# Kernel tuning notes

Measured on AMD Instinct MI355X. Metric: run time of the kernel, lower is better.

## Reference

```python
import jax, jax.numpy as jnp
import numpy as np

NUM_HEADS = 32
NUM_KV_HEADS = 8
HEAD_DIM = 64

def rotate_half(x):
    x1, x2 = jnp.split(x, 2, axis=-1)
    return jnp.concatenate((-x2, x1), axis=-1)

def setup_inputs() -> dict:
    key = jax.random.key(0)
    ks = jax.random.split(key, 7)
    B, S, H = 1, 2048, 2048
    hidden_states = jax.random.normal(ks[0], (B, S, H), dtype=jnp.float32)
    # RoPE tables (llama-style) for positions 0..S-1
    inv_freq = 1.0 / (10000.0 ** (np.arange(0, HEAD_DIM, 2, dtype=np.float32) / HEAD_DIM))
    t = np.arange(S, dtype=np.float32)
    freqs = np.outer(t, inv_freq)              # [S, HEAD_DIM//2]
    emb = np.concatenate([freqs, freqs], axis=-1)  # [S, HEAD_DIM]
    cos = jnp.asarray(np.cos(emb)[None], dtype=jnp.float32)  # [1, S, HEAD_DIM]
    sin = jnp.asarray(np.sin(emb)[None], dtype=jnp.float32)
    sc = 0.02
    Wq = jax.random.normal(ks[1], (H, H), dtype=jnp.float32) * sc
    Wk = jax.random.normal(ks[2], (NUM_KV_HEADS * HEAD_DIM, H), dtype=jnp.float32) * sc
    Wv = jax.random.normal(ks[3], (NUM_KV_HEADS * HEAD_DIM, H), dtype=jnp.float32) * sc
    Wo = jax.random.normal(ks[4], (H, H), dtype=jnp.float32) * sc
    return {"hidden_states": hidden_states, "cos": cos, "sin": sin,
            "Wq": Wq, "Wk": Wk, "Wv": Wv, "Wo": Wo}

def reference(hidden_states, cos, sin, Wq, Wk, Wv, Wo):
    B, S, H = hidden_states.shape
    nh, nkv, hd = NUM_HEADS, NUM_KV_HEADS, HEAD_DIM
    n_rep = nh // nkv
    # projections (torch Linear: x @ W.T)
    q = (hidden_states @ Wq.T).reshape(B, S, nh, hd).transpose(0, 2, 1, 3)   # [B,nh,S,hd]
    k = (hidden_states @ Wk.T).reshape(B, S, nkv, hd).transpose(0, 2, 1, 3)  # [B,nkv,S,hd]
    v = (hidden_states @ Wv.T).reshape(B, S, nkv, hd).transpose(0, 2, 1, 3)
    # RoPE: cos/sin [B,S,hd] -> broadcast over heads
    c = cos[:, None, :, :]
    s = sin[:, None, :, :]
    q = q * c + rotate_half(q) * s
    k = k * c + rotate_half(k) * s
    # GQA: repeat_interleave kv heads
    k = jnp.repeat(k, n_rep, axis=1)  # [B,nh,S,hd]
    v = jnp.repeat(v, n_rep, axis=1)
    # eager attention (NOTE: source applies no causal mask)
    scores = jnp.einsum('bhqd,bhkd->bhqk', q, k) / jnp.sqrt(jnp.float32(hd))
    attn = jax.nn.softmax(scores.astype(jnp.float32), axis=-1).astype(q.dtype)
    out = jnp.einsum('bhqk,bhkd->bhqd', attn, v)          # [B,nh,S,hd]
    out = out.transpose(0, 2, 1, 3).reshape(B, S, nh * hd)
    return out @ Wo.T
```

## Files before the change

### kernel.cpp

```cpp
#include <hip/hip_runtime.h>

typedef __bf16 bf16;
typedef __bf16 bf16x8 __attribute__((ext_vector_type(8)));
typedef __bf16 bf16x4 __attribute__((ext_vector_type(4)));
typedef float f32x4 __attribute__((ext_vector_type(4)));

__device__ __forceinline__ void gload_lds16(const void* g, void* l) {
  __builtin_amdgcn_global_load_lds(
      (const __attribute__((address_space(1))) void*)g,
      (__attribute__((address_space(3))) void*)l, 16, 0, 0);
}

__global__ __launch_bounds__(256) void cast_f32_bf16(const float* __restrict__ src,
                                                     bf16* __restrict__ dst, int n) {
  int i = (blockIdx.x * 256 + threadIdx.x) * 4;
  if (i >= n) return;
  float4 v = *(const float4*)(src + i);
  bf16x4 o;
  o[0] = (bf16)v.x; o[1] = (bf16)v.y; o[2] = (bf16)v.z; o[3] = (bf16)v.w;
  *(bf16x4*)(dst + i) = o;
}

__global__ __launch_bounds__(256) void gemm_qkv(const bf16* __restrict__ A,
                                                const bf16* __restrict__ B,
                                                bf16* __restrict__ QK,
                                                bf16* __restrict__ Vt_g,
                                                int K) {
  __shared__ bf16 As[128][64];
  __shared__ bf16 Bs[128][64];
  const int tid  = threadIdx.x;
  const int lane = tid & 63;
  const int w    = tid >> 6;
  const int m0 = blockIdx.y * 128;
  const int n0 = blockIdx.x * 128;
  const int wr = w >> 1, wc = w & 1;

  f32x4 acc[4][4] = {};

  const bf16* Ag = A + (long)(m0 + w * 32 + (lane >> 3)) * K + ((lane & 7) << 3);
  const bf16* Bg = B + (long)(n0 + w * 32 + (lane >> 3)) * K + ((lane & 7) << 3);

  for (int k0 = 0; k0 < K; k0 += 64) {
#pragma unroll
    for (int i = 0; i < 4; ++i) {
      gload_lds16(Ag + (long)i * 8 * K + k0, &As[w * 32 + i * 8][0]);
      gload_lds16(Bg + (long)i * 8 * K + k0, &Bs[w * 32 + i * 8][0]);
    }
    __syncthreads();
#pragma unroll
    for (int kk = 0; kk < 64; kk += 32) {
      bf16x8 a[4], b[4];
#pragma unroll
      for (int m = 0; m < 4; ++m)
        a[m] = *(const bf16x8*)&As[wr * 64 + m * 16 + (lane & 15)][kk + ((lane >> 4) << 3)];
#pragma unroll
      for (int n = 0; n < 4; ++n)
        b[n] = *(const bf16x8*)&Bs[wc * 64 + n * 16 + (lane & 15)][kk + ((lane >> 4) << 3)];
#pragma unroll
      for (int m = 0; m < 4; ++m)
#pragma unroll
        for (int n = 0; n < 4; ++n)
          acc[m][n] = __builtin_amdgcn_mfma_f32_16x16x32_bf16(a[m], b[n], acc[m][n], 0, 0, 0);
    }
    __syncthreads();
  }

  const int rb = m0 + wr * 64 + ((lane >> 4) << 2);
  const int cb = n0 + wc * 64 + (lane & 15);
  if (n0 >= 2560) {
#pragma unroll
    for (int m = 0; m < 4; ++m)
#pragma unroll
      for (int n = 0; n < 4; ++n)
#pragma unroll
        for (int j = 0; j < 4; ++j)
          Vt_g[(long)(cb + n * 16 - 2560) * 2048 + (rb + m * 16 + j)] = (bf16)acc[m][n][j];
  } else {
#pragma unroll
    for (int m = 0; m < 4; ++m)
#pragma unroll
      for (int n = 0; n < 4; ++n)
#pragma unroll
        for (int j = 0; j < 4; ++j)
          QK[(long)(rb + m * 16 + j) * 2560 + (cb + n * 16)] = (bf16)acc[m][n][j];
  }
}

__global__ __launch_bounds__(256) void gemm_bt_f32(const bf16* __restrict__ A,
                                                   const bf16* __restrict__ B,
                                                   float* __restrict__ C,
                                                   int K, int ldc) {
  __shared__ bf16 As[128][64];
  __shared__ bf16 Bs[128][64];
  const int tid  = threadIdx.x;
  const int lane = tid & 63;
  const int w    = tid >> 6;
  const int m0 = blockIdx.y * 128;
  const int n0 = blockIdx.x * 128;
  const int wr = w >> 1, wc = w & 1;

  f32x4 acc[4][4] = {};

  const bf16* Ag = A + (long)(m0 + w * 32 + (lane >> 3)) * K + ((lane & 7) << 3);
  const bf16* Bg = B + (long)(n0 + w * 32 + (lane >> 3)) * K + ((lane & 7) << 3);

  for (int k0 = 0; k0 < K; k0 += 64) {
#pragma unroll
    for (int i = 0; i < 4; ++i) {
      gload_lds16(Ag + (long)i * 8 * K + k0, &As[w * 32 + i * 8][0]);
      gload_lds16(Bg + (long)i * 8 * K + k0, &Bs[w * 32 + i * 8][0]);
    }
    __syncthreads();
#pragma unroll
    for (int kk = 0; kk < 64; kk += 32) {
      bf16x8 a[4], b[4];
#pragma unroll
      for (int m = 0; m < 4; ++m)
        a[m] = *(const bf16x8*)&As[wr * 64 + m * 16 + (lane & 15)][kk + ((lane >> 4) << 3)];
#pragma unroll
      for (int n = 0; n < 4; ++n)
        b[n] = *(const bf16x8*)&Bs[wc * 64 + n * 16 + (lane & 15)][kk + ((lane >> 4) << 3)];
#pragma unroll
      for (int m = 0; m < 4; ++m)
#pragma unroll
        for (int n = 0; n < 4; ++n)
          acc[m][n] = __builtin_amdgcn_mfma_f32_16x16x32_bf16(a[m], b[n], acc[m][n], 0, 0, 0);
    }
    __syncthreads();
  }

  const int rb = m0 + wr * 64 + ((lane >> 4) << 2);
  const int cb = n0 + wc * 64 + (lane & 15);
#pragma unroll
  for (int m = 0; m < 4; ++m)
#pragma unroll
    for (int n = 0; n < 4; ++n)
#pragma unroll
      for (int j = 0; j < 4; ++j)
        C[(long)(rb + m * 16 + j) * ldc + (cb + n * 16)] = acc[m][n][j];
}

__global__ __launch_bounds__(256) void rope_scale(bf16* __restrict__ QK,
                                                  const float* __restrict__ cosb,
                                                  const float* __restrict__ sinb) {
  int t = blockIdx.x * 256 + threadIdx.x;
  int s = t / 160;
  int rem = t - s * 160;
  int hh = rem >> 2;
  int d0 = (rem & 3) << 3;
  long base = (long)s * 2560 + hh * 64 + d0;
  bf16x8 lo = *(const bf16x8*)(QK + base);
  bf16x8 hi = *(const bf16x8*)(QK + base + 32);
  float4 c0 = *(const float4*)(cosb + s * 64 + d0);
  float4 c1 = *(const float4*)(cosb + s * 64 + d0 + 4);
  float4 s0 = *(const float4*)(sinb + s * 64 + d0);
  float4 s1 = *(const float4*)(sinb + s * 64 + d0 + 4);
  float cs[8] = {c0.x, c0.y, c0.z, c0.w, c1.x, c1.y, c1.z, c1.w};
  float sn[8] = {s0.x, s0.y, s0.z, s0.w, s1.x, s1.y, s1.z, s1.w};
  float scale = hh < 32 ? 0.125f : 1.0f;
  bf16x8 nlo, nhi;
#pragma unroll
  for (int i = 0; i < 8; ++i) {
    float L = (float)lo[i], H = (float)hi[i];
    nlo[i] = (bf16)((L * cs[i] - H * sn[i]) * scale);
    nhi[i] = (bf16)((H * cs[i] + L * sn[i]) * scale);
  }
  *(bf16x8*)(QK + base)      = nlo;
  *(bf16x8*)(QK + base + 32) = nhi;
}

__global__ __launch_bounds__(512) void attn_v2(const bf16* __restrict__ QK,
                                               const bf16* __restrict__ Vg,
                                               bf16* __restrict__ O) {
  constexpr int LDT = 72;
  __shared__ bf16 Kt[64][LDT];
  __shared__ bf16 Vt[64][LDT];
  __shared__ bf16 Pl[8][16][LDT];
  const int h   = blockIdx.y;
  const int q0  = blockIdx.x * 128;
  const int kvh = h >> 2;
  const int tid = threadIdx.x, lane = tid & 63, w = tid >> 6;
  const int l15 = lane & 15, lq = lane >> 4;

  const bf16* qptr = QK + (long)(q0 + w * 16 + l15) * 2560 + h * 64 + (lq << 3);
  bf16x8 qf[2];
  qf[0] = *(const bf16x8*)(qptr);
  qf[1] = *(const bf16x8*)(qptr + 32);

  const int sr = tid >> 3;
  const int sc = (tid & 7) << 3;
  const bf16* ksrc = QK + (long)sr * 2560 + 2048 + kvh * 64 + sc;
  const bf16* vsrc = Vg + (long)(kvh * 64 + sr) * 2048 + sc;

  f32x4 oacc[4] = {};
  float lrow[4] = {0.f, 0.f, 0.f, 0.f};

  bf16x8 kreg = *(const bf16x8*)ksrc;
  bf16x8 vreg = *(const bf16x8*)vsrc;

  for (int t = 0; t < 32; ++t) {
    *(bf16x8*)&Kt[sr][sc] = kreg;
    *(bf16x8*)&Vt[sr][sc] = vreg;
    __syncthreads();
    if (t != 31) {
      ksrc += 64 * 2560;
      vsrc += 64;
      kreg = *(const bf16x8*)ksrc;
      vreg = *(const bf16x8*)vsrc;
    }

    f32x4 sacc[4] = {};
#pragma unroll
    for (int kx = 0; kx < 2; ++kx)
#pragma unroll
      for (int nf = 0; nf < 4; ++nf) {
        bf16x8 b = *(const bf16x8*)&Kt[nf * 16 + l15][kx * 32 + (lq << 3)];
        sacc[nf] = __builtin_amdgcn_mfma_f32_16x16x32_bf16(qf[kx], b, sacc[nf], 0, 0, 0);
      }

#pragma unroll
    for (int nf = 0; nf < 4; ++nf)
#pragma unroll
      for (int j = 0; j < 4; ++j) {
        float pv = __expf(sacc[nf][j]);
        lrow[j] += pv;
        Pl[w][(lq << 2) + j][nf * 16 + l15] = (bf16)pv;
      }

#pragma unroll
    for (int kx = 0; kx < 2; ++kx) {
      bf16x8 a = *(const bf16x8*)&Pl[w][l15][kx * 32 + (lq << 3)];
#pragma unroll
      for (int nf = 0; nf < 4; ++nf) {
        bf16x8 b = *(const bf16x8*)&Vt[nf * 16 + l15][kx * 32 + (lq << 3)];
        oacc[nf] = __builtin_amdgcn_mfma_f32_16x16x32_bf16(a, b, oacc[nf], 0, 0, 0);
      }
    }
    __syncthreads();
  }

  float ls[4];
#pragma unroll
  for (int j = 0; j < 4; ++j) {
    float v = lrow[j];
#pragma unroll
    for (int off = 1; off < 16; off <<= 1) v += __shfl_xor(v, off, 64);
    ls[j] = v;
  }
#pragma unroll
  for (int nf = 0; nf < 4; ++nf)
#pragma unroll
    for (int j = 0; j < 4; ++j) {
      int r = q0 + w * 16 + (lq << 2) + j;
      int c = h * 64 + nf * 16 + l15;
      O[(long)r * 2048 + c] = (bf16)(oacc[nf][j] / ls[j]);
    }
}

extern "C" void kernel_launch(void* const* d_in, const int* in_sizes, int n_in,
                              void* d_out, int out_size, void* d_ws, size_t ws_size,
                              hipStream_t stream) {
  const float* hs   = (const float*)d_in[0];
  const float* cosb = (const float*)d_in[1];
  const float* sinb = (const float*)d_in[2];
  const float* Wq   = (const float*)d_in[3];
  const float* Wk   = (const float*)d_in[4];
  const float* Wv   = (const float*)d_in[5];
  const float* Wo   = (const float*)d_in[6];
  float* out = (float*)d_out;

  char* ws = (char*)d_ws;
  bf16* hsb   = (bf16*)(ws);
  bf16* Wqkv  = (bf16*)(ws + (8l  << 20));
  bf16* Wob   = (bf16*)(ws + (20l << 20));
  bf16* QKbuf = (bf16*)(ws + (28l << 20));
  bf16* Vt_g  = (bf16*)(ws + (38l << 20));
  bf16* AO    = (bf16*)(ws + (40l << 20));

  cast_f32_bf16<<<4096, 256, 0, stream>>>(hs, hsb, 4194304);
  cast_f32_bf16<<<4096, 256, 0, stream>>>(Wq, Wqkv, 4194304);
  cast_f32_bf16<<<1024, 256, 0, stream>>>(Wk, Wqkv + 2048l * 2048, 1048576);
  cast_f32_bf16<<<1024, 256, 0, stream>>>(Wv, Wqkv + 2560l * 2048, 1048576);
  cast_f32_bf16<<<4096, 256, 0, stream>>>(Wo, Wob, 4194304);

  gemm_qkv<<<dim3(24, 16), 256, 0, stream>>>(hsb, Wqkv, QKbuf, Vt_g, 2048);

  rope_scale<<<1280, 256, 0, stream>>>(QKbuf, cosb, sinb);

  attn_v2<<<dim3(16, 32), 512, 0, stream>>>(QKbuf, Vt_g, AO);

  gemm_bt_f32<<<dim3(16, 16), 256, 0, stream>>>(AO, Wob, out, 2048, 2048);
}
```

Before: 271.7 us.

## Fuse casts into one kernel, fold RoPE into QKV GEMM, double-buffer GEMM LDS

The five separate f32-to-bf16 cast launches become one kernel that picks its source and destination by index range. The RoPE and scale pass is moved into the QKV GEMM epilogue, which removes one launch and a read-modify-write of the QK buffer. Both GEMMs now double-buffer their LDS tiles so the next K-slice load is issued before the current slice's MFMAs. The cost is twice the LDS per block, which may lower occupancy, and scattered scalar cos/sin loads in the epilogue.

Measured after the change: 260.2 us. 1.04x faster.

```diff
diff --git a/kernel.cpp b/kernel.cpp
--- a/kernel.cpp
+++ b/kernel.cpp
@@ -11,51 +11,74 @@
       (__attribute__((address_space(3))) void*)l, 16, 0, 0);
 }
 
-__global__ __launch_bounds__(256) void cast_f32_bf16(const float* __restrict__ src,
-                                                     bf16* __restrict__ dst, int n) {
-  int i = (blockIdx.x * 256 + threadIdx.x) * 4;
-  if (i >= n) return;
-  float4 v = *(const float4*)(src + i);
+__global__ __launch_bounds__(256) void cast_all(const float* __restrict__ hs,
+                                                const float* __restrict__ Wq,
+                                                const float* __restrict__ Wk,
+                                                const float* __restrict__ Wv,
+                                                const float* __restrict__ Wo,
+                                                bf16* __restrict__ hsb,
+                                                bf16* __restrict__ Wqkv,
+                                                bf16* __restrict__ Wob) {
+  long i = (long)blockIdx.x * 256 + threadIdx.x;
+  const float* s; bf16* d;
+  if (i < 1048576)      { s = hs + i * 4;                 d = hsb  + i * 4; }
+  else if (i < 2097152) { s = Wq + (i - 1048576) * 4;     d = Wqkv + (i - 1048576) * 4; }
+  else if (i < 2359296) { s = Wk + (i - 2097152) * 4;     d = Wqkv + 4194304 + (i - 2097152) * 4; }
+  else if (i < 2621440) { s = Wv + (i - 2359296) * 4;     d = Wqkv + 5242880 + (i - 2359296) * 4; }
+  else                  { s = Wo + (i - 2621440) * 4;     d = Wob  + (i - 2621440) * 4; }
+  float4 v = *(const float4*)s;
   bf16x4 o;
   o[0] = (bf16)v.x; o[1] = (bf16)v.y; o[2] = (bf16)v.z; o[3] = (bf16)v.w;
-  *(bf16x4*)(dst + i) = o;
+  *(bf16x4*)d = o;
 }
 
 __global__ __launch_bounds__(256) void gemm_qkv(const bf16* __restrict__ A,
                                                 const bf16* __restrict__ B,
+                                                const float* __restrict__ cosb,
+                                                const float* __restrict__ sinb,
                                                 bf16* __restrict__ QK,
                                                 bf16* __restrict__ Vt_g,
                                                 int K) {
-  __shared__ bf16 As[128][64];
-  __shared__ bf16 Bs[128][64];
+  __shared__ bf16 As[2][128][64];
+  __shared__ bf16 Bs[2][128][64];
   const int tid  = threadIdx.x;
   const int lane = tid & 63;
   const int w    = tid >> 6;
   const int m0 = blockIdx.y * 128;
   const int n0 = blockIdx.x * 128;
   const int wr = w >> 1, wc = w & 1;
+  const int l15 = lane & 15, lq = lane >> 4;
 
   f32x4 acc[4][4] = {};
 
   const bf16* Ag = A + (long)(m0 + w * 32 + (lane >> 3)) * K + ((lane & 7) << 3);
   const bf16* Bg = B + (long)(n0 + w * 32 + (lane >> 3)) * K + ((lane & 7) << 3);
 
+#pragma unroll
+  for (int i = 0; i < 4; ++i) {
+    gload_lds16(Ag + (long)i * 8 * K, &As[0][w * 32 + i * 8][0]);
+    gload_lds16(Bg + (long)i * 8 * K, &Bs[0][w * 32 + i * 8][0]);
+  }
+  __syncthreads();
+
+  int cur = 0;
   for (int k0 = 0; k0 < K; k0 += 64) {
-#pragma unroll
-    for (int i = 0; i < 4; ++i) {
-      gload_lds16(Ag + (long)i * 8 * K + k0, &As[w * 32 + i * 8][0]);
-      gload_lds16(Bg + (long)i * 8 * K + k0, &Bs[w * 32 + i * 8][0]);
-    }
-    __syncthreads();
+    if (k0 + 64 < K) {
+#pragma unroll
+      for (int i = 0; i < 4; ++i) {
+        gload_lds16(Ag + (long)i * 8 * K + k0 + 64, &As[cur ^ 1][w * 32 + i * 8][0]);
+        gload_lds16(Bg + (long)i * 8 * K + k0 + 64, &Bs[cur ^ 1][w * 32 + i * 8][0]);
+      }
+    }
 #pragma unroll
     for (int kk = 0; kk < 64; kk += 32) {
       bf16x8 a[4], b[4];
 #pragma unroll
       for (int m = 0; m < 4; ++m)
-        a[m] = *(const bf16x8*)&As[wr * 64 + m * 16 + (lane & 15)][kk + ((lane >> 4) << 3)];
+        a[m] = *(const bf16x8*)&As[cur][wr * 64 + m * 16 + l15][kk + (lq << 3)];
 #pragma unroll
       for (int n = 0; n < 4; ++n)
-        b[n] = *(const bf16x8*)&Bs[wc * 64 + n * 16 + (lane & 15)][kk + ((lane >> 4) << 3)];
+        b[n] = *(const bf16x8*)&Bs[cur][wc * 64 + n * 16 + l15][kk + (lq << 3)];
 #pragma unroll
       for (int m = 0; m < 4; ++m)
 #pragma unroll
@@ -63,11 +86,12 @@
           acc[m][n] = __builtin_amdgcn_mfma_f32_16x16x32_bf16(a[m], b[n], acc[m][n], 0, 0, 0);
     }
     __syncthreads();
-  }
-
-  const int rb = m0 + wr * 64 + ((lane >> 4) << 2);
-  const int cb = n0 + wc * 64 + (lane & 15);
+    cur ^= 1;
+  }
+
+  const int rb = m0 + wr * 64 + (lq << 2);
   if (n0 >= 2560) {
+    const int cb = n0 + wc * 64 + l15;
 #pragma unroll
     for (int m = 0; m < 4; ++m)
 #pragma unroll
@@ -76,13 +100,25 @@
         for (int j = 0; j < 4; ++j)
           Vt_g[(long)(cb + n * 16 - 2560) * 2048 + (rb + m * 16 + j)] = (bf16)acc[m][n][j];
   } else {
+    const int colb = n0 + wc * 64;
+    const float scale = (colb >> 6) < 32 ? 0.125f : 1.0f;
 #pragma unroll
     for (int m = 0; m < 4; ++m)
 #pragma unroll
-      for (int n = 0; n < 4; ++n)
-#pragma unroll
-        for (int j = 0; j < 4; ++j)
-          QK[(long)(rb + m * 16 + j) * 2560 + (cb + n * 16)] = (bf16)acc[m][n][j];
+      for (int j = 0; j < 4; ++j) {
+        const int r = rb + m * 16 + j;
+        const float* cp = cosb + (long)r * 64;
+        const float* sp = sinb + (long)r * 64;
+        bf16* qrow = QK + (long)r * 2560 + colb;
+#pragma unroll
+        for (int n = 0; n < 2; ++n) {
+          const int d = n * 16 + l15;
+          float c = cp[d], s = sp[d];
+          float L = acc[m][n][j], H = acc[m][n + 2][j];
+          qrow[d]      = (bf16)((L * c - H * s) * scale);
+          qrow[d + 32] = (bf16)((H * c + L * s) * scale);
+        }
+      }
   }
 }
 
@@ -90,36 +126,46 @@
                                                    const bf16* __restrict__ B,
                                                    float* __restrict__ C,
                                                    int K, int ldc) {
-  __shared__ bf16 As[128][64];
-  __shared__ bf16 Bs[128][64];
+  __shared__ bf16 As[2][128][64];
+  __shared__ bf16 Bs[2][128][64];
   const int tid  = threadIdx.x;
   const int lane = tid & 63;
   const int w    = tid >> 6;
   const int m0 = blockIdx.y * 128;
   const int n0 = blockIdx.x * 128;
   const int wr = w >> 1, wc = w & 1;
+  const int l15 = lane & 15, lq = lane >> 4;
 
   f32x4 acc[4][4] = {};
 
   const bf16* Ag = A + (long)(m0 + w * 32 + (lane >> 3)) * K + ((lane & 7) << 3);
   const bf16* Bg = B + (long)(n0 + w * 32 + (lane >> 3)) * K + ((lane & 7) << 3);
 
+#pragma unroll
+  for (int i = 0; i < 4; ++i) {
+    gload_lds16(Ag + (long)i * 8 * K, &As[0][w * 32 + i * 8][0]);
+    gload_lds16(Bg + (long)i * 8 * K, &Bs[0][w * 32 + i * 8][0]);
+  }
+  __syncthreads();
+
+  int cur = 0;
   for (int k0 = 0; k0 < K; k0 += 64) {
-#pragma unroll
-    for (int i = 0; i < 4; ++i) {
-      gload_lds16(Ag + (long)i * 8 * K + k0, &As[w * 32 + i * 8][0]);
-      gload_lds16(Bg + (long)i * 8 * K + k0, &Bs[w * 32 + i * 8][0]);
-    }
-    __syncthreads();
+    if (k0 + 64 < K) {
+#pragma unroll
+      for (int i = 0; i < 4; ++i) {
+        gload_lds16(Ag + (long)i * 8 * K + k0 + 64, &As[cur ^ 1][w * 32 + i * 8][0]);
+        gload_lds16(Bg + (long)i * 8 * K + k0 + 64, &Bs[cur ^ 1][w * 32 + i * 8][0]);
+      }
+    }
 #pragma unroll
     for (int kk = 0; kk < 64; kk += 32) {
       bf16x8 a[4], b[4];
 #pragma unroll
       for (int m = 0; m < 4; ++m)
-        a[m] = *(const bf16x8*)&As[wr * 64 + m * 16 + (lane & 15)][kk + ((lane >> 4) << 3)];
+        a[m] = *(const bf16x8*)&As[cur][wr * 64 + m * 16 + l15][kk + (lq << 3)];
 #pragma unroll
       for (int n = 0; n < 4; ++n)
-        b[n] = *(const bf16x8*)&Bs[wc * 64 + n * 16 + (lane & 15)][kk + ((lane >> 4) << 3)];
+        b[n] = *(const bf16x8*)&Bs[cur][wc * 64 + n * 16 + l15][kk + (lq << 3)];
 #pragma unroll
       for (int m = 0; m < 4; ++m)
 #pragma unroll
@@ -127,10 +173,11 @@
           acc[m][n] = __builtin_amdgcn_mfma_f32_16x16x32_bf16(a[m], b[n], acc[m][n], 0, 0, 0);
     }
     __syncthreads();
-  }
-
-  const int rb = m0 + wr * 64 + ((lane >> 4) << 2);
-  const int cb = n0 + wc * 64 + (lane & 15);
+    cur ^= 1;
+  }
+
+  const int rb = m0 + wr * 64 + (lq << 2);
+  const int cb = n0 + wc * 64 + l15;
 #pragma unroll
   for (int m = 0; m < 4; ++m)
 #pragma unroll
@@ -138,35 +185,6 @@
 #pragma unroll
       for (int j = 0; j < 4; ++j)
         C[(long)(rb + m * 16 + j) * ldc + (cb + n * 16)] = acc[m][n][j];
-}
-
-__global__ __launch_bounds__(256) void rope_scale(bf16* __restrict__ QK,
-                                                  const float* __restrict__ cosb,
-                                                  const float* __restrict__ sinb) {
-  int t = blockIdx.x * 256 + threadIdx.x;
-  int s = t / 160;
-  int rem = t - s * 160;
-  int hh = rem >> 2;
-  int d0 = (rem & 3) << 3;
-  long base = (long)s * 2560 + hh * 64 + d0;
-  bf16x8 lo = *(const bf16x8*)(QK + base);
-  bf16x8 hi = *(const bf16x8*)(QK + base + 32);
-  float4 c0 = *(const float4*)(cosb + s * 64 + d0);
-  float4 c1 = *(const float4*)(cosb + s * 64 + d0 + 4);
-  float4 s0 = *(const float4*)(sinb + s * 64 + d0);
-  float4 s1 = *(const float4*)(sinb + s * 64 + d0 + 4);
-  float cs[8] = {c0.x, c0.y, c0.z, c0.w, c1.x, c1.y, c1.z, c1.w};
-  float sn[8] = {s0.x, s0.y, s0.z, s0.w, s1.x, s1.y, s1.z, s1.w};
-  float scale = hh < 32 ? 0.125f : 1.0f;
-  bf16x8 nlo, nhi;
-#pragma unroll
-  for (int i = 0; i < 8; ++i) {
-    float L = (float)lo[i], H = (float)hi[i];
-    nlo[i] = (bf16)((L * cs[i] - H * sn[i]) * scale);
-    nhi[i] = (bf16)((H * cs[i] + L * sn[i]) * scale);
-  }
-  *(bf16x8*)(QK + base)      = nlo;
-  *(bf16x8*)(QK + base + 32) = nhi;
 }
 
 __global__ __launch_bounds__(512) void attn_v2(const bf16* __restrict__ QK,
@@ -277,15 +295,9 @@
   bf16* Vt_g  = (bf16*)(ws + (38l << 20));
   bf16* AO    = (bf16*)(ws + (40l << 20));
 
-  cast_f32_bf16<<<4096, 256, 0, stream>>>(hs, hsb, 4194304);
-  cast_f32_bf16<<<4096, 256, 0, stream>>>(Wq, Wqkv, 4194304);
-  cast_f32_bf16<<<1024, 256, 0, stream>>>(Wk, Wqkv + 2048l * 2048, 1048576);
-  cast_f32_bf16<<<1024, 256, 0, stream>>>(Wv, Wqkv + 2560l * 2048, 1048576);
-  cast_f32_bf16<<<4096, 256, 0, stream>>>(Wo, Wob, 4194304);
-
-  gemm_qkv<<<dim3(24, 16), 256, 0, stream>>>(hsb, Wqkv, QKbuf, Vt_g, 2048);
-
-  rope_scale<<<1280, 256, 0, stream>>>(QKbuf, cosb, sinb);
+  cast_all<<<14336, 256, 0, stream>>>(hs, Wq, Wk, Wv, Wo, hsb, Wqkv, Wob);
+
+  gemm_qkv<<<dim3(24, 16), 256, 0, stream>>>(hsb, Wqkv, cosb, sinb, QKbuf, Vt_g, 2048);
 
   attn_v2<<<dim3(16, 32), 512, 0, stream>>>(QKbuf, Vt_g, AO);
 
```
